# Performance work log

Measured on AMD Instinct MI355X. Metric: run time of the kernel, lower is better.

## Reference

```python
import jax, jax.numpy as jnp
import numpy as np

B, S, D, K = 8, 2048, 1024, 256
LN_EPS = 1e-5


def _freq_positions(input_dim, num_freq, spec_len):
    # torch.linspace(0, input_dim//2, num_freq).long(), clamped to rfft length
    pos = np.linspace(0.0, input_dim // 2, num_freq).astype(np.int64)
    return np.clip(pos, 0, spec_len - 1)


def setup_inputs() -> dict:
    key = jax.random.key(0)
    k1, k2, k3 = jax.random.split(key, 3)
    x = jax.random.normal(k1, (B, S, D), dtype=jnp.float32)
    # magnitude init: init_magnitude=0.1 (small jitter keeps gradients non-degenerate)
    magnitude = 0.1 + 0.01 * jax.random.normal(k2, (K, D), dtype=jnp.float32)
    phase = 0.1 * jax.random.normal(k3, (K, D), dtype=jnp.float32)
    interference_w = 0.01 * jax.random.normal(jax.random.fold_in(key, 7), (K, K), dtype=jnp.float32)
    ln_gamma = jnp.ones((D,), dtype=jnp.float32)
    ln_beta = jnp.zeros((D,), dtype=jnp.float32)
    return {"x": x, "magnitude": magnitude, "phase": phase,
            "interference_w": interference_w, "ln_gamma": ln_gamma, "ln_beta": ln_beta}


def reference(x, magnitude, phase, interference_w, ln_gamma, ln_beta):
    b, s, d = x.shape
    residual = x
    padded_len = 1 << int(np.ceil(np.log2(s)))  # static
    if padded_len > s:
        x = jnp.pad(x, ((0, 0), (0, padded_len - s), (0, 0)))
    # FFT along sequence axis: (B, padded_len//2+1, D) complex
    x_fft = jnp.fft.rfft(x, axis=1)
    freq_pos = _freq_positions(d, magnitude.shape[0], x_fft.shape[1])  # (K,) static ints

    # gather selected frequencies: (B, K, D)
    x_selected = x_fft[:, freq_pos, :]
    # complex weights from magnitude/phase
    cw = (magnitude * jnp.cos(phase) + 1j * magnitude * jnp.sin(phase)).astype(jnp.complex64)
    x_weighted = x_selected * cw[None, :, :]
    # interference on real part: bkd,kj->bjd
    interference = jnp.einsum('bkd,kj->bjd', jnp.real(x_weighted), interference_w)
    x_processed = x_weighted + 0.1 * interference.astype(jnp.complex64)

    # scatter back (positions are unique for these dims)
    x_fft_processed = x_fft.at[:, freq_pos, :].set(x_processed)
    x_rec = jnp.fft.irfft(x_fft_processed, n=padded_len, axis=1)[:, :s, :]

    # residual + LayerNorm over last dim (dropout is identity in eval)
    y = x_rec + residual
    mu = jnp.mean(y, axis=-1, keepdims=True)
    var = jnp.mean(jnp.square(y - mu), axis=-1, keepdims=True)
    y = (y - mu) * jax.lax.rsqrt(var + LN_EPS)
    return y * ln_gamma + ln_beta
```

## Files before the change

kernel.cpp:

```cpp
#include <hip/hip_runtime.h>
#include <math.h>

#define NS 2048
#define ND 1024
#define NK 256
#define NB 8

typedef __attribute__((ext_vector_type(8))) short short8;
typedef __attribute__((ext_vector_type(4))) float f32x4;
typedef __attribute__((ext_vector_type(4))) unsigned short u16x4;
typedef __attribute__((ext_vector_type(8))) unsigned short u16x8;

__device__ __forceinline__ unsigned short f2bf(float x) {
  unsigned int u = __float_as_uint(x);
  u = (u + 0x7fffu + ((u >> 16) & 1u)) >> 16;
  return (unsigned short)u;
}
__device__ __forceinline__ float bf2f(unsigned short h) {
  return __uint_as_float(((unsigned int)h) << 16);
}

__device__ __forceinline__ int fpos(int k) {
  return (k == 255) ? 512 : (int)((float)k * (512.0f / 255.0f));
}

__global__ __launch_bounds__(256) void k_tab(unsigned short* __restrict__ CF,
                                             unsigned short* __restrict__ CS) {
  int gid = blockIdx.x * 256 + threadIdx.x;
  if (gid < 512 * 2048) {
    int m = gid >> 11, s = gid & 2047;
    int ph = (fpos(m & 255) * s) & 2047;
    float th = (float)ph * 0.0030679615757712823f;
    float v = (m < 256) ? cosf(th) : -sinf(th);
    CF[gid] = f2bf(v);
  } else {
    int g = gid - 512 * 2048;
    int s = g >> 9, kk = g & 511;
    int ph = (fpos(kk & 255) * s) & 2047;
    float th = (float)ph * 0.0030679615757712823f;
    float v = (kk < 256) ? cosf(th) : -sinf(th);
    CS[g] = f2bf(v);
  }
}

__global__ __launch_bounds__(256) void k_cw(const float* __restrict__ mag,
                                            const float* __restrict__ ph,
                                            float* __restrict__ mc,
                                            float* __restrict__ ms) {
  int i = blockIdx.x * 256 + threadIdx.x;
  float m = mag[i], p = ph[i];
  float sp, cp;
  sincosf(p, &sp, &cp);
  mc[i] = m * cp;
  ms[i] = m * sp;
}

__global__ __launch_bounds__(256) void k_conv(const float* __restrict__ x,
                                              unsigned short* __restrict__ xt) {
  int bid = blockIdx.x;
  int b = bid >> 9, rem = bid & 511;
  int s0 = (rem >> 4) * 64, d0 = (rem & 15) * 64;
  int t = threadIdx.x;
  __shared__ __attribute__((aligned(16))) unsigned short lt[64 * 72];
#pragma unroll
  for (int c = 0; c < 4; c++) {
    int e = c * 256 + t;
    int row = e >> 4, col = (e & 15) * 4;
    float4 v = *(const float4*)&x[((size_t)b * NS + s0 + row) * ND + d0 + col];
    lt[(col + 0) * 72 + row] = f2bf(v.x);
    lt[(col + 1) * 72 + row] = f2bf(v.y);
    lt[(col + 2) * 72 + row] = f2bf(v.z);
    lt[(col + 3) * 72 + row] = f2bf(v.w);
  }
  __syncthreads();
  int dl = t >> 2, sc = (t & 3) * 16;
  u16x8 a = *(u16x8*)&lt[dl * 72 + sc];
  u16x8 bb = *(u16x8*)&lt[dl * 72 + sc + 8];
  size_t o = ((size_t)b * ND + d0 + dl) * NS + s0 + sc;
  *(u16x8*)&xt[o] = a;
  *(u16x8*)&xt[o + 8] = bb;
}

template <int BM, int BN, int OUTBF>
__global__ __launch_bounds__(256) void gemm_tt(const unsigned short* __restrict__ A,
                                               const unsigned short* __restrict__ B,
                                               void* __restrict__ C,
                                               int M, int N, int K) {
  constexpr int MI = BM / 32, NI = BN / 32;
  constexpr int ACH = BM / 32, BCH = BN / 32;
  const int mt = M / BM, nt = N / BN;
  int bid = blockIdx.x;
  int b = bid / (mt * nt);
  int r = bid % (mt * nt);
  int m0 = (r / nt) * BM, n0 = (r % nt) * BN;
  int t = threadIdx.x, lane = t & 63;
  int wr = (t >> 7) & 1, wc = (t >> 6) & 1;
  __shared__ __attribute__((aligned(16))) unsigned short As[BM * 64];
  __shared__ __attribute__((aligned(16))) unsigned short Bs[BN * 64];

  const unsigned short* Ag = A + (size_t)m0 * K;
  const unsigned short* Bg = B + ((size_t)b * N + n0) * K;

  f32x4 acc[MI][NI];
#pragma unroll
  for (int i = 0; i < MI; i++)
#pragma unroll
    for (int j = 0; j < NI; j++) acc[i][j] = {0.f, 0.f, 0.f, 0.f};

  short8 la[ACH], lb[BCH], na[ACH], nb[BCH];

#pragma unroll
  for (int c = 0; c < ACH; c++) {
    int e = c * 256 + t, row = e >> 3, sl = e & 7;
    la[c] = *(const short8*)&Ag[(size_t)row * K + sl * 8];
  }
#pragma unroll
  for (int c = 0; c < BCH; c++) {
    int e = c * 256 + t, row = e >> 3, sl = e & 7;
    lb[c] = *(const short8*)&Bg[(size_t)row * K + sl * 8];
  }

  const int nkt = K / 64;
  for (int kt = 0; kt < nkt; ++kt) {
    if (kt + 1 < nkt) {
      int k0 = (kt + 1) * 64;
#pragma unroll
      for (int c = 0; c < ACH; c++) {
        int e = c * 256 + t, row = e >> 3, sl = e & 7;
        na[c] = *(const short8*)&Ag[(size_t)row * K + k0 + sl * 8];
      }
#pragma unroll
      for (int c = 0; c < BCH; c++) {
        int e = c * 256 + t, row = e >> 3, sl = e & 7;
        nb[c] = *(const short8*)&Bg[(size_t)row * K + k0 + sl * 8];
      }
    }
    __syncthreads();
#pragma unroll
    for (int c = 0; c < ACH; c++) {
      int e = c * 256 + t, row = e >> 3, sl = e & 7;
      *(short8*)&As[row * 64 + ((sl ^ (row & 7)) * 8)] = la[c];
    }
#pragma unroll
    for (int c = 0; c < BCH; c++) {
      int e = c * 256 + t, row = e >> 3, sl = e & 7;
      *(short8*)&Bs[row * 64 + ((sl ^ (row & 7)) * 8)] = lb[c];
    }
    __syncthreads();
#pragma unroll
    for (int ks = 0; ks < 2; ks++) {
      short8 af[MI], bfr[NI];
#pragma unroll
      for (int mi = 0; mi < MI; mi++) {
        int rowl = wr * (BM / 2) + mi * 16 + (lane & 15);
        int sl = ks * 4 + (lane >> 4);
        af[mi] = *(const short8*)&As[rowl * 64 + ((sl ^ (rowl & 7)) * 8)];
      }
#pragma unroll
      for (int ni = 0; ni < NI; ni++) {
        int rowl = wc * (BN / 2) + ni * 16 + (lane & 15);
        int sl = ks * 4 + (lane >> 4);
        bfr[ni] = *(const short8*)&Bs[rowl * 64 + ((sl ^ (rowl & 7)) * 8)];
      }
#pragma unroll
      for (int mi = 0; mi < MI; mi++)
#pragma unroll
        for (int ni = 0; ni < NI; ni++)
          acc[mi][ni] = __builtin_amdgcn_mfma_f32_16x16x32_bf16(
              af[mi], bfr[ni], acc[mi][ni], 0, 0, 0);
    }
#pragma unroll
    for (int c = 0; c < ACH; c++) la[c] = na[c];
#pragma unroll
    for (int c = 0; c < BCH; c++) lb[c] = nb[c];
  }

#pragma unroll
  for (int mi = 0; mi < MI; mi++) {
#pragma unroll
    for (int ni = 0; ni < NI; ni++) {
      int row0 = m0 + wr * (BM / 2) + mi * 16 + ((lane >> 4) * 4);
      int col = n0 + wc * (BN / 2) + ni * 16 + (lane & 15);
#pragma unroll
      for (int q = 0; q < 4; q++) {
        size_t o = ((size_t)b * M + row0 + q) * (size_t)N + col;
        if (OUTBF)
          ((unsigned short*)C)[o] = f2bf(acc[mi][ni][q]);
        else
          ((float*)C)[o] = acc[mi][ni][q];
      }
    }
  }
}

__global__ __launch_bounds__(256) void k1b(const unsigned short* __restrict__ Xq,
                                           const float* __restrict__ mc,
                                           const float* __restrict__ ms,
                                           unsigned short* __restrict__ RXw) {
  int e8 = blockIdx.x * 256 + threadIdx.x;
  int d8 = (e8 & 127) * 8;
  int rowg = e8 >> 7;
  int b = rowg >> 8, k = rowg & 255;
  u16x8 re = *(const u16x8*)&Xq[((size_t)b * 512 + k) * ND + d8];
  u16x8 im = *(const u16x8*)&Xq[((size_t)b * 512 + 256 + k) * ND + d8];
  u16x8 o;
#pragma unroll
  for (int q = 0; q < 8; q++) {
    float mcv = mc[k * ND + d8 + q], msv = ms[k * ND + d8 + q];
    o[q] = f2bf(mcv * bf2f(re[q]) - msv * bf2f(im[q]));
  }
  *(u16x8*)&RXw[(size_t)rowg * ND + d8] = o;
}

__global__ __launch_bounds__(256) void k2_intf(const float* __restrict__ W,
                                               const unsigned short* __restrict__ RXw,
                                               const unsigned short* __restrict__ Xq,
                                               const float* __restrict__ mc,
                                               const float* __restrict__ ms,
                                               unsigned short* __restrict__ DltT) {
  int bid = blockIdx.x;
  int b = bid >> 6, rem = bid & 63;
  int jt = rem >> 4, dt = rem & 15;
  int t = threadIdx.x;
  int tj = t >> 4, td = t & 15;
  __shared__ __attribute__((aligned(16))) unsigned short Rx[256 * 64];
  __shared__ __attribute__((aligned(16))) unsigned short Wl[256 * 64];
#pragma unroll
  for (int c = 0; c < 8; c++) {
    int e = c * 256 + t, row = e >> 3, col = (e & 7) * 8;
    *(u16x8*)&Rx[row * 64 + col] =
        *(const u16x8*)&RXw[((size_t)b * NK + row) * ND + dt * 64 + col];
  }
#pragma unroll
  for (int c = 0; c < 16; c++) {
    int e = c * 256 + t, row = e >> 4, col = (e & 15) * 4;
    float4 w = *(const float4*)&W[row * NK + jt * 64 + col];
    u16x4 wv = {f2bf(w.x), f2bf(w.y), f2bf(w.z), f2bf(w.w)};
    *(u16x4*)&Wl[row * 64 + col] = wv;
  }
  __syncthreads();
  float acc[4][4];
#pragma unroll
  for (int i = 0; i < 4; i++)
#pragma unroll
    for (int j = 0; j < 4; j++) acc[i][j] = 0.f;
#pragma unroll 4
  for (int k = 0; k < 256; k++) {
    u16x4 r4 = *(const u16x4*)&Rx[k * 64 + td * 4];
    u16x4 w4 = *(const u16x4*)&Wl[k * 64 + tj * 4];
    float rf[4] = {bf2f(r4[0]), bf2f(r4[1]), bf2f(r4[2]), bf2f(r4[3])};
    float wf[4] = {bf2f(w4[0]), bf2f(w4[1]), bf2f(w4[2]), bf2f(w4[3])};
#pragma unroll
    for (int jj = 0; jj < 4; jj++)
#pragma unroll
      for (int q = 0; q < 4; q++) acc[jj][q] = fmaf(wf[jj], rf[q], acc[jj][q]);
  }
  int jbase = jt * 64 + tj * 4;
  jbase = jt * 64 + tj * 4;
  int dg = dt * 64 + td * 4;
  float dre[4][4], dim[4][4];
#pragma unroll
  for (int jj = 0; jj < 4; jj++) {
    int j = jbase + jj;
    float alpha = ((j == 0) ? 1.0f : 2.0f) * (1.0f / 2048.0f);
    u16x4 re4 = *(const u16x4*)&Xq[((size_t)b * 512 + j) * ND + dg];
    u16x4 im4 = *(const u16x4*)&Xq[((size_t)b * 512 + 256 + j) * ND + dg];
    float4 mc4 = *(const float4*)&mc[j * ND + dg];
    float4 ms4 = *(const float4*)&ms[j * ND + dg];
    float mcc[4] = {mc4.x, mc4.y, mc4.z, mc4.w};
    float mss[4] = {ms4.x, ms4.y, ms4.z, ms4.w};
#pragma unroll
    for (int q = 0; q < 4; q++) {
      float xr = bf2f(re4[q]), xi = bf2f(im4[q]);
      float m1 = mcc[q] - 1.0f;
      dre[jj][q] = alpha * (m1 * xr - mss[q] * xi + 0.1f * acc[jj][q]);
      dim[jj][q] = alpha * (mss[q] * xr + m1 * xi);
    }
  }
#pragma unroll
  for (int q = 0; q < 4; q++) {
    u16x4 vr = {f2bf(dre[0][q]), f2bf(dre[1][q]), f2bf(dre[2][q]), f2bf(dre[3][q])};
    u16x4 vi = {f2bf(dim[0][q]), f2bf(dim[1][q]), f2bf(dim[2][q]), f2bf(dim[3][q])};
    size_t rowo = ((size_t)b * ND + dg + q) * 512;
    *(u16x4*)&DltT[rowo + jbase] = vr;
    *(u16x4*)&DltT[rowo + 256 + jbase] = vi;
  }
}

__global__ __launch_bounds__(256) void k4_ln(const float* __restrict__ x,
                                             const float* __restrict__ g,
                                             const float* __restrict__ be,
                                             float* __restrict__ out) {
  int row = blockIdx.x;
  int t = threadIdx.x;
  size_t base = (size_t)row * ND + t * 4;
  float4 cv = *(float4*)&out[base];
  float4 xv = *(const float4*)&x[base];
  float v[4] = {fmaf(2.f, xv.x, cv.x), fmaf(2.f, xv.y, cv.y),
                fmaf(2.f, xv.z, cv.z), fmaf(2.f, xv.w, cv.w)};
  float s = v[0] + v[1] + v[2] + v[3];
  float q = v[0] * v[0] + v[1] * v[1] + v[2] * v[2] + v[3] * v[3];
#pragma unroll
  for (int o = 32; o >= 1; o >>= 1) {
    s += __shfl_xor(s, o, 64);
    q += __shfl_xor(q, o, 64);
  }
  __shared__ float ss[4], qs[4];
  if ((t & 63) == 0) { ss[t >> 6] = s; qs[t >> 6] = q; }
  __syncthreads();
  s = ss[0] + ss[1] + ss[2] + ss[3];
  q = qs[0] + qs[1] + qs[2] + qs[3];
  float mu = s * (1.0f / (float)ND);
  float var = q * (1.0f / (float)ND) - mu * mu;
  float rstd = rsqrtf(var + 1e-5f);
  float4 gv = *(const float4*)&g[t * 4];
  float4 bv = *(const float4*)&be[t * 4];
  float4 ov;
  ov.x = (v[0] - mu) * rstd * gv.x + bv.x;
  ov.y = (v[1] - mu) * rstd * gv.y + bv.y;
  ov.z = (v[2] - mu) * rstd * gv.z + bv.z;
  ov.w = (v[3] - mu) * rstd * gv.w + bv.w;
  *(float4*)&out[base] = ov;
}

extern "C" void kernel_launch(void* const* d_in, const int* in_sizes, int n_in,
                              void* d_out, int out_size, void* d_ws, size_t ws_size,
                              hipStream_t stream) {
  const float* x   = (const float*)d_in[0];
  const float* mag = (const float*)d_in[1];
  const float* ph  = (const float*)d_in[2];
  const float* W   = (const float*)d_in[3];
  const float* g   = (const float*)d_in[4];
  const float* be  = (const float*)d_in[5];
  float* out = (float*)d_out;
  char* o = (char*)d_out;
  char* w = (char*)d_ws;

  unsigned short* CF  = (unsigned short*)w;
  unsigned short* CS  = (unsigned short*)(w + (2u << 20));
  float* mc           = (float*)(w + (4u << 20));
  float* ms           = (float*)(w + (5u << 20));
  unsigned short* Dlt = (unsigned short*)(w + (6u << 20));
  unsigned short* xt  = (unsigned short*)o;
  unsigned short* Xq  = (unsigned short*)(o + (32u << 20));
  unsigned short* RXw = (unsigned short*)(o + (40u << 20));

  k_tab<<<8192, 256, 0, stream>>>(CF, CS);
  k_cw<<<1024, 256, 0, stream>>>(mag, ph, mc, ms);
  k_conv<<<4096, 256, 0, stream>>>(x, xt);
  gemm_tt<128, 64, 1><<<512, 256, 0, stream>>>(CF, xt, Xq, 512, 1024, 2048);
  k1b<<<1024, 256, 0, stream>>>(Xq, mc, ms, RXw);
  k2_intf<<<512, 256, 0, stream>>>(W, RXw, Xq, mc, ms, Dlt);
  gemm_tt<128, 128, 0><<<1024, 256, 0, stream>>>(CS, Dlt, out, 2048, 1024, 512);
  k4_ln<<<16384, 256, 0, stream>>>(x, g, be, out);
}
```

Measured before the change: 242.3 us.

## Transpose spectral intermediates, use MFMA for interference, direct-to-LDS GEMM loads

Reorganizes the pipeline so the forward DFT GEMM writes its output transposed (d-major), with the weight tables and interference matrix pre-transposed to match. The scalar FMA interference kernel is replaced by an MFMA GEMM plus a separate elementwise kernel. The GEMM is rewritten to use global_load_lds instead of register staging, which drops the XOR swizzle and the software prefetch. The inverse GEMM now writes a bf16 correction buffer rather than fp32, which cuts memory traffic but adds rounding error, and the unswizzled LDS layout may cause bank conflicts.

```diff
diff --git a/kernel.cpp b/kernel.cpp
--- a/kernel.cpp
+++ b/kernel.cpp
@@ -22,6 +22,12 @@
 
 __device__ __forceinline__ int fpos(int k) {
   return (k == 255) ? 512 : (int)((float)k * (512.0f / 255.0f));
+}
+
+__device__ __forceinline__ void gll16(const unsigned short* g, unsigned short* l) {
+  __builtin_amdgcn_global_load_lds(
+      (__attribute__((address_space(1))) void*)(void*)const_cast<unsigned short*>(g),
+      (__attribute__((address_space(3))) void*)l, 16, 0, 0);
 }
 
 __global__ __launch_bounds__(256) void k_tab(unsigned short* __restrict__ CF,
@@ -43,16 +49,64 @@
   }
 }
 
-__global__ __launch_bounds__(256) void k_cw(const float* __restrict__ mag,
-                                            const float* __restrict__ ph,
-                                            float* __restrict__ mc,
-                                            float* __restrict__ ms) {
-  int i = blockIdx.x * 256 + threadIdx.x;
-  float m = mag[i], p = ph[i];
-  float sp, cp;
-  sincosf(p, &sp, &cp);
-  mc[i] = m * cp;
-  ms[i] = m * sp;
+__global__ __launch_bounds__(256) void k_cwT(const float* __restrict__ mag,
+                                             const float* __restrict__ ph,
+                                             float* __restrict__ mcT,
+                                             float* __restrict__ msT) {
+  int bid = blockIdx.x;
+  int kt = bid >> 4, dt = bid & 15;
+  int t = threadIdx.x;
+  __shared__ float lc[64][68], ls[64][68];
+  int kl = t >> 4, d4 = (t & 15) * 4;
+#pragma unroll
+  for (int i = 0; i < 4; i++) {
+    int k = i * 16 + kl;
+    size_t off = (size_t)(kt * 64 + k) * ND + dt * 64 + d4;
+    float4 mg = *(const float4*)&mag[off];
+    float4 pp = *(const float4*)&ph[off];
+    float m[4] = {mg.x, mg.y, mg.z, mg.w}, p[4] = {pp.x, pp.y, pp.z, pp.w};
+#pragma unroll
+    for (int q = 0; q < 4; q++) {
+      float sp, cp;
+      sincosf(p[q], &sp, &cp);
+      lc[k][d4 + q] = m[q] * cp;
+      ls[k][d4 + q] = m[q] * sp;
+    }
+  }
+  __syncthreads();
+  int dl = t >> 2, kc = (t & 3) * 16;
+#pragma unroll
+  for (int i = 0; i < 16; i += 4) {
+    float4 vc = {lc[kc + i][dl], lc[kc + i + 1][dl], lc[kc + i + 2][dl], lc[kc + i + 3][dl]};
+    float4 vs = {ls[kc + i][dl], ls[kc + i + 1][dl], ls[kc + i + 2][dl], ls[kc + i + 3][dl]};
+    size_t o = (size_t)(dt * 64 + dl) * 256 + kt * 64 + kc + i;
+    *(float4*)&mcT[o] = vc;
+    *(float4*)&msT[o] = vs;
+  }
+}
+
+__global__ __launch_bounds__(256) void k_wt(const float* __restrict__ W,
+                                            unsigned short* __restrict__ WT) {
+  int bid = blockIdx.x;
+  int kt = bid >> 2, jt = bid & 3;
+  int t = threadIdx.x;
+  __shared__ float lw[64][68];
+  int kl = t >> 4, j4 = (t & 15) * 4;
+#pragma unroll
+  for (int i = 0; i < 4; i++) {
+    int k = i * 16 + kl;
+    float4 wv = *(const float4*)&W[(size_t)(kt * 64 + k) * 256 + jt * 64 + j4];
+    lw[k][j4 + 0] = wv.x; lw[k][j4 + 1] = wv.y;
+    lw[k][j4 + 2] = wv.z; lw[k][j4 + 3] = wv.w;
+  }
+  __syncthreads();
+  int jl = t >> 2, kc = (t & 3) * 16;
+#pragma unroll
+  for (int i = 0; i < 16; i += 4) {
+    u16x4 v = {f2bf(lw[kc + i][jl]), f2bf(lw[kc + i + 1][jl]),
+               f2bf(lw[kc + i + 2][jl]), f2bf(lw[kc + i + 3][jl])};
+    *(u16x4*)&WT[(size_t)(jt * 64 + jl) * 256 + kt * 64 + kc + i] = v;
+  }
 }
 
 __global__ __launch_bounds__(256) void k_conv(const float* __restrict__ x,
@@ -81,25 +135,24 @@
   *(u16x8*)&xt[o + 8] = bb;
 }
 
-template <int BM, int BN, int OUTBF>
-__global__ __launch_bounds__(256) void gemm_tt(const unsigned short* __restrict__ A,
-                                               const unsigned short* __restrict__ B,
-                                               void* __restrict__ C,
-                                               int M, int N, int K) {
+template <int BM, int BN, int OUTT>
+__global__ __launch_bounds__(256) void gemm97(const unsigned short* __restrict__ A,
+                                              const unsigned short* __restrict__ B,
+                                              unsigned short* __restrict__ C,
+                                              int M, int N, int K,
+                                              size_t sA, size_t sB) {
   constexpr int MI = BM / 32, NI = BN / 32;
-  constexpr int ACH = BM / 32, BCH = BN / 32;
   const int mt = M / BM, nt = N / BN;
   int bid = blockIdx.x;
-  int b = bid / (mt * nt);
-  int r = bid % (mt * nt);
+  int b = bid / (mt * nt), r = bid % (mt * nt);
   int m0 = (r / nt) * BM, n0 = (r % nt) * BN;
-  int t = threadIdx.x, lane = t & 63;
+  int t = threadIdx.x, lane = t & 63, w = t >> 6;
   int wr = (t >> 7) & 1, wc = (t >> 6) & 1;
   __shared__ __attribute__((aligned(16))) unsigned short As[BM * 64];
   __shared__ __attribute__((aligned(16))) unsigned short Bs[BN * 64];
-
-  const unsigned short* Ag = A + (size_t)m0 * K;
-  const unsigned short* Bg = B + ((size_t)b * N + n0) * K;
+  const unsigned short* Ag = A + b * sA + (size_t)m0 * K;
+  const unsigned short* Bg = B + b * sB + (size_t)n0 * K;
+  int arow = lane >> 3, ak = (lane & 7) * 8;
 
   f32x4 acc[MI][NI];
 #pragma unroll
@@ -107,72 +160,40 @@
 #pragma unroll
     for (int j = 0; j < NI; j++) acc[i][j] = {0.f, 0.f, 0.f, 0.f};
 
-  short8 la[ACH], lb[BCH], na[ACH], nb[BCH];
-
-#pragma unroll
-  for (int c = 0; c < ACH; c++) {
-    int e = c * 256 + t, row = e >> 3, sl = e & 7;
-    la[c] = *(const short8*)&Ag[(size_t)row * K + sl * 8];
-  }
-#pragma unroll
-  for (int c = 0; c < BCH; c++) {
-    int e = c * 256 + t, row = e >> 3, sl = e & 7;
-    lb[c] = *(const short8*)&Bg[(size_t)row * K + sl * 8];
-  }
-
-  const int nkt = K / 64;
-  for (int kt = 0; kt < nkt; ++kt) {
-    if (kt + 1 < nkt) {
-      int k0 = (kt + 1) * 64;
-#pragma unroll
-      for (int c = 0; c < ACH; c++) {
-        int e = c * 256 + t, row = e >> 3, sl = e & 7;
-        na[c] = *(const short8*)&Ag[(size_t)row * K + k0 + sl * 8];
+  for (int kt = 0; kt < K / 64; kt++) {
+    int kofs = kt * 64;
+#pragma unroll
+    for (int i = 0; i < BM / 32; i++) {
+      int r0 = w * (BM / 4) + i * 8;
+      gll16(Ag + (size_t)(r0 + arow) * K + kofs + ak, &As[r0 * 64]);
+    }
+#pragma unroll
+    for (int i = 0; i < BN / 32; i++) {
+      int r0 = w * (BN / 4) + i * 8;
+      gll16(Bg + (size_t)(r0 + arow) * K + kofs + ak, &Bs[r0 * 64]);
+    }
+    __syncthreads();
+#pragma unroll
+    for (int ks = 0; ks < 2; ks++) {
+      short8 af[MI], bfv[NI];
+#pragma unroll
+      for (int mi = 0; mi < MI; mi++) {
+        int row = wr * (BM / 2) + mi * 16 + (lane & 15);
+        af[mi] = *(const short8*)&As[row * 64 + (ks * 4 + (lane >> 4)) * 8];
       }
 #pragma unroll
-      for (int c = 0; c < BCH; c++) {
-        int e = c * 256 + t, row = e >> 3, sl = e & 7;
-        nb[c] = *(const short8*)&Bg[(size_t)row * K + k0 + sl * 8];
-      }
-    }
-    __syncthreads();
-#pragma unroll
-    for (int c = 0; c < ACH; c++) {
-      int e = c * 256 + t, row = e >> 3, sl = e & 7;
-      *(short8*)&As[row * 64 + ((sl ^ (row & 7)) * 8)] = la[c];
-    }
-#pragma unroll
-    for (int c = 0; c < BCH; c++) {
-      int e = c * 256 + t, row = e >> 3, sl = e & 7;
-      *(short8*)&Bs[row * 64 + ((sl ^ (row & 7)) * 8)] = lb[c];
-    }
-    __syncthreads();
-#pragma unroll
-    for (int ks = 0; ks < 2; ks++) {
-      short8 af[MI], bfr[NI];
-#pragma unroll
-      for (int mi = 0; mi < MI; mi++) {
-        int rowl = wr * (BM / 2) + mi * 16 + (lane & 15);
-        int sl = ks * 4 + (lane >> 4);
-        af[mi] = *(const short8*)&As[rowl * 64 + ((sl ^ (rowl & 7)) * 8)];
-      }
-#pragma unroll
       for (int ni = 0; ni < NI; ni++) {
-        int rowl = wc * (BN / 2) + ni * 16 + (lane & 15);
-        int sl = ks * 4 + (lane >> 4);
-        bfr[ni] = *(const short8*)&Bs[rowl * 64 + ((sl ^ (rowl & 7)) * 8)];
+        int row = wc * (BN / 2) + ni * 16 + (lane & 15);
+        bfv[ni] = *(const short8*)&Bs[row * 64 + (ks * 4 + (lane >> 4)) * 8];
       }
 #pragma unroll
       for (int mi = 0; mi < MI; mi++)
 #pragma unroll
         for (int ni = 0; ni < NI; ni++)
           acc[mi][ni] = __builtin_amdgcn_mfma_f32_16x16x32_bf16(
-              af[mi], bfr[ni], acc[mi][ni], 0, 0, 0);
-    }
-#pragma unroll
-    for (int c = 0; c < ACH; c++) la[c] = na[c];
-#pragma unroll
-    for (int c = 0; c < BCH; c++) lb[c] = nb[c];
+              af[mi], bfv[ni], acc[mi][ni], 0, 0, 0);
+    }
+    __syncthreads();
   }
 
 #pragma unroll
@@ -181,123 +202,86 @@
     for (int ni = 0; ni < NI; ni++) {
       int row0 = m0 + wr * (BM / 2) + mi * 16 + ((lane >> 4) * 4);
       int col = n0 + wc * (BN / 2) + ni * 16 + (lane & 15);
-#pragma unroll
-      for (int q = 0; q < 4; q++) {
-        size_t o = ((size_t)b * M + row0 + q) * (size_t)N + col;
-        if (OUTBF)
-          ((unsigned short*)C)[o] = f2bf(acc[mi][ni][q]);
-        else
-          ((float*)C)[o] = acc[mi][ni][q];
+      if (OUTT == 1) {
+        u16x4 v = {f2bf(acc[mi][ni][0]), f2bf(acc[mi][ni][1]),
+                   f2bf(acc[mi][ni][2]), f2bf(acc[mi][ni][3])};
+        *(u16x4*)&C[((size_t)b * N + col) * M + row0] = v;
+      } else {
+#pragma unroll
+        for (int q = 0; q < 4; q++)
+          C[((size_t)b * M + row0 + q) * N + col] = f2bf(acc[mi][ni][q]);
       }
     }
   }
 }
 
-__global__ __launch_bounds__(256) void k1b(const unsigned short* __restrict__ Xq,
-                                           const float* __restrict__ mc,
-                                           const float* __restrict__ ms,
-                                           unsigned short* __restrict__ RXw) {
-  int e8 = blockIdx.x * 256 + threadIdx.x;
-  int d8 = (e8 & 127) * 8;
-  int rowg = e8 >> 7;
-  int b = rowg >> 8, k = rowg & 255;
-  u16x8 re = *(const u16x8*)&Xq[((size_t)b * 512 + k) * ND + d8];
-  u16x8 im = *(const u16x8*)&Xq[((size_t)b * 512 + 256 + k) * ND + d8];
+__global__ __launch_bounds__(256) void k1bT(const unsigned short* __restrict__ XqT,
+                                            const float* __restrict__ mcT,
+                                            const float* __restrict__ msT,
+                                            unsigned short* __restrict__ RXwT) {
+  int gid = blockIdx.x * 256 + threadIdx.x;
+  int rw = gid >> 5;
+  int k0 = (gid & 31) * 8;
+  int d = rw & 1023;
+  u16x8 re = *(const u16x8*)&XqT[(size_t)rw * 512 + k0];
+  u16x8 im = *(const u16x8*)&XqT[(size_t)rw * 512 + 256 + k0];
+  float4 c0 = *(const float4*)&mcT[d * 256 + k0];
+  float4 c1 = *(const float4*)&mcT[d * 256 + k0 + 4];
+  float4 s0 = *(const float4*)&msT[d * 256 + k0];
+  float4 s1 = *(const float4*)&msT[d * 256 + k0 + 4];
+  float cc[8] = {c0.x, c0.y, c0.z, c0.w, c1.x, c1.y, c1.z, c1.w};
+  float ss[8] = {s0.x, s0.y, s0.z, s0.w, s1.x, s1.y, s1.z, s1.w};
   u16x8 o;
 #pragma unroll
+  for (int q = 0; q < 8; q++)
+    o[q] = f2bf(cc[q] * bf2f(re[q]) - ss[q] * bf2f(im[q]));
+  *(u16x8*)&RXwT[(size_t)rw * 256 + k0] = o;
+}
+
+__global__ __launch_bounds__(256) void k2b(const unsigned short* __restrict__ IT,
+                                           const unsigned short* __restrict__ XqT,
+                                           const float* __restrict__ mcT,
+                                           const float* __restrict__ msT,
+                                           unsigned short* __restrict__ DltT) {
+  int gid = blockIdx.x * 256 + threadIdx.x;
+  int rw = gid >> 5;
+  int j0 = (gid & 31) * 8;
+  int d = rw & 1023;
+  u16x8 iv = *(const u16x8*)&IT[(size_t)rw * 256 + j0];
+  u16x8 re = *(const u16x8*)&XqT[(size_t)rw * 512 + j0];
+  u16x8 im = *(const u16x8*)&XqT[(size_t)rw * 512 + 256 + j0];
+  float4 c0 = *(const float4*)&mcT[d * 256 + j0];
+  float4 c1 = *(const float4*)&mcT[d * 256 + j0 + 4];
+  float4 s0 = *(const float4*)&msT[d * 256 + j0];
+  float4 s1 = *(const float4*)&msT[d * 256 + j0 + 4];
+  float cc[8] = {c0.x, c0.y, c0.z, c0.w, c1.x, c1.y, c1.z, c1.w};
+  float ss[8] = {s0.x, s0.y, s0.z, s0.w, s1.x, s1.y, s1.z, s1.w};
+  u16x8 orv, oiv;
+#pragma unroll
   for (int q = 0; q < 8; q++) {
-    float mcv = mc[k * ND + d8 + q], msv = ms[k * ND + d8 + q];
-    o[q] = f2bf(mcv * bf2f(re[q]) - msv * bf2f(im[q]));
-  }
-  *(u16x8*)&RXw[(size_t)rowg * ND + d8] = o;
-}
-
-__global__ __launch_bounds__(256) void k2_intf(const float* __restrict__ W,
-                                               const unsigned short* __restrict__ RXw,
-                                               const unsigned short* __restrict__ Xq,
-                                               const float* __restrict__ mc,
-                                               const float* __restrict__ ms,
-                                               unsigned short* __restrict__ DltT) {
-  int bid = blockIdx.x;
-  int b = bid >> 6, rem = bid & 63;
-  int jt = rem >> 4, dt = rem & 15;
-  int t = threadIdx.x;
-  int tj = t >> 4, td = t & 15;
-  __shared__ __attribute__((aligned(16))) unsigned short Rx[256 * 64];
-  __shared__ __attribute__((aligned(16))) unsigned short Wl[256 * 64];
-#pragma unroll
-  for (int c = 0; c < 8; c++) {
-    int e = c * 256 + t, row = e >> 3, col = (e & 7) * 8;
-    *(u16x8*)&Rx[row * 64 + col] =
-        *(const u16x8*)&RXw[((size_t)b * NK + row) * ND + dt * 64 + col];
-  }
-#pragma unroll
-  for (int c = 0; c < 16; c++) {
-    int e = c * 256 + t, row = e >> 4, col = (e & 15) * 4;
-    float4 w = *(const float4*)&W[row * NK + jt * 64 + col];
-    u16x4 wv = {f2bf(w.x), f2bf(w.y), f2bf(w.z), f2bf(w.w)};
-    *(u16x4*)&Wl[row * 64 + col] = wv;
-  }
-  __syncthreads();
-  float acc[4][4];
-#pragma unroll
-  for (int i = 0; i < 4; i++)
-#pragma unroll
-    for (int j = 0; j < 4; j++) acc[i][j] = 0.f;
-#pragma unroll 4
-  for (int k = 0; k < 256; k++) {
-    u16x4 r4 = *(const u16x4*)&Rx[k * 64 + td * 4];
-    u16x4 w4 = *(const u16x4*)&Wl[k * 64 + tj * 4];
-    float rf[4] = {bf2f(r4[0]), bf2f(r4[1]), bf2f(r4[2]), bf2f(r4[3])};
-    float wf[4] = {bf2f(w4[0]), bf2f(w4[1]), bf2f(w4[2]), bf2f(w4[3])};
-#pragma unroll
-    for (int jj = 0; jj < 4; jj++)
-#pragma unroll
-      for (int q = 0; q < 4; q++) acc[jj][q] = fmaf(wf[jj], rf[q], acc[jj][q]);
-  }
-  int jbase = jt * 64 + tj * 4;
-  jbase = jt * 64 + tj * 4;
-  int dg = dt * 64 + td * 4;
-  float dre[4][4], dim[4][4];
-#pragma unroll
-  for (int jj = 0; jj < 4; jj++) {
-    int j = jbase + jj;
+    int j = j0 + q;
     float alpha = ((j == 0) ? 1.0f : 2.0f) * (1.0f / 2048.0f);
-    u16x4 re4 = *(const u16x4*)&Xq[((size_t)b * 512 + j) * ND + dg];
-    u16x4 im4 = *(const u16x4*)&Xq[((size_t)b * 512 + 256 + j) * ND + dg];
-    float4 mc4 = *(const float4*)&mc[j * ND + dg];
-    float4 ms4 = *(const float4*)&ms[j * ND + dg];
-    float mcc[4] = {mc4.x, mc4.y, mc4.z, mc4.w};
-    float mss[4] = {ms4.x, ms4.y, ms4.z, ms4.w};
-#pragma unroll
-    for (int q = 0; q < 4; q++) {
-      float xr = bf2f(re4[q]), xi = bf2f(im4[q]);
-      float m1 = mcc[q] - 1.0f;
-      dre[jj][q] = alpha * (m1 * xr - mss[q] * xi + 0.1f * acc[jj][q]);
-      dim[jj][q] = alpha * (mss[q] * xr + m1 * xi);
-    }
-  }
-#pragma unroll
-  for (int q = 0; q < 4; q++) {
-    u16x4 vr = {f2bf(dre[0][q]), f2bf(dre[1][q]), f2bf(dre[2][q]), f2bf(dre[3][q])};
-    u16x4 vi = {f2bf(dim[0][q]), f2bf(dim[1][q]), f2bf(dim[2][q]), f2bf(dim[3][q])};
-    size_t rowo = ((size_t)b * ND + dg + q) * 512;
-    *(u16x4*)&DltT[rowo + jbase] = vr;
-    *(u16x4*)&DltT[rowo + 256 + jbase] = vi;
-  }
+    float xr = bf2f(re[q]), xi = bf2f(im[q]), ii = bf2f(iv[q]);
+    float m1 = cc[q] - 1.0f;
+    orv[q] = f2bf(alpha * (m1 * xr - ss[q] * xi + 0.1f * ii));
+    oiv[q] = f2bf(alpha * (ss[q] * xr + m1 * xi));
+  }
+  *(u16x8*)&DltT[(size_t)rw * 512 + j0] = orv;
+  *(u16x8*)&DltT[(size_t)rw * 512 + 256 + j0] = oiv;
 }
 
 __global__ __launch_bounds__(256) void k4_ln(const float* __restrict__ x,
+                                             const unsigned short* __restrict__ corr,
                                              const float* __restrict__ g,
                                              const float* __restrict__ be,
                                              float* __restrict__ out) {
   int row = blockIdx.x;
   int t = threadIdx.x;
   size_t base = (size_t)row * ND + t * 4;
-  float4 cv = *(float4*)&out[base];
+  u16x4 cv = *(const u16x4*)&corr[base];
   float4 xv = *(const float4*)&x[base];
-  float v[4] = {fmaf(2.f, xv.x, cv.x), fmaf(2.f, xv.y, cv.y),
-                fmaf(2.f, xv.z, cv.z), fmaf(2.f, xv.w, cv.w)};
+  float v[4] = {fmaf(2.f, xv.x, bf2f(cv[0])), fmaf(2.f, xv.y, bf2f(cv[1])),
+                fmaf(2.f, xv.z, bf2f(cv[2])), fmaf(2.f, xv.w, bf2f(cv[3]))};
   float s = v[0] + v[1] + v[2] + v[3];
   float q = v[0] * v[0] + v[1] * v[1] + v[2] * v[2] + v[3] * v[3];
 #pragma unroll
@@ -333,24 +317,31 @@
   const float* g   = (const float*)d_in[4];
   const float* be  = (const float*)d_in[5];
   float* out = (float*)d_out;
-  char* o = (char*)d_out;
   char* w = (char*)d_ws;
 
-  unsigned short* CF  = (unsigned short*)w;
-  unsigned short* CS  = (unsigned short*)(w + (2u << 20));
-  float* mc           = (float*)(w + (4u << 20));
-  float* ms           = (float*)(w + (5u << 20));
-  unsigned short* Dlt = (unsigned short*)(w + (6u << 20));
-  unsigned short* xt  = (unsigned short*)o;
-  unsigned short* Xq  = (unsigned short*)(o + (32u << 20));
-  unsigned short* RXw = (unsigned short*)(o + (40u << 20));
+  unsigned short* CF   = (unsigned short*)(w);
+  unsigned short* CS   = (unsigned short*)(w + (2ull << 20));
+  float*          mcT  = (float*)(w + (4ull << 20));
+  float*          msT  = (float*)(w + (5ull << 20));
+  unsigned short* WT   = (unsigned short*)(w + (6ull << 20));
+  unsigned short* XqT  = (unsigned short*)(w + (7ull << 20));
+  unsigned short* RXwT = (unsigned short*)(w + (15ull << 20));
+  unsigned short* IT   = (unsigned short*)(w + (19ull << 20));
+  unsigned short* DltT = (unsigned short*)(w + (23ull << 20));
+  unsigned short* corr = (unsigned short*)(w + (31ull << 20));
+  unsigned short* xt   = (unsigned short*)(w + (63ull << 20));
 
   k_tab<<<8192, 256, 0, stream>>>(CF, CS);
-  k_cw<<<1024, 256, 0, stream>>>(mag, ph, mc, ms);
+  k_cwT<<<64, 256, 0, stream>>>(mag, ph, mcT, msT);
+  k_wt<<<16, 256, 0, stream>>>(W, WT);
   k_conv<<<4096, 256, 0, stream>>>(x, xt);
-  gemm_tt<128, 64, 1><<<512, 256, 0, stream>>>(CF, xt, Xq, 512, 1024, 2048);
-  k1b<<<1024, 256, 0, stream>>>(Xq, mc, ms, RXw);
-  k2_intf<<<512, 256, 0, stream>>>(W, RXw, Xq, mc, ms, Dlt);
-  gemm_tt<128, 128, 0><<<1024, 256, 0, stream>>>(CS, Dlt, out, 2048, 1024, 512);
-  k4_ln<<<16384, 256, 0, stream>>>(x, g, be, out);
-}
+  gemm97<128, 64, 1><<<512, 256, 0, stream>>>(CF, xt, XqT, 512, 1024, 2048,
+                                              0, (size_t)1024 * 2048);
+  k1bT<<<1024, 256, 0, stream>>>(XqT, mcT, msT, RXwT);
+  gemm97<128, 64, 0><<<256, 256, 0, stream>>>(RXwT, WT, IT, 1024, 256, 256,
+                                              (size_t)1024 * 256, 0);
+  k2b<<<1024, 256, 0, stream>>>(IT, XqT, mcT, msT, DltT);
+  gemm97<128, 128, 0><<<1024, 256, 0, stream>>>(CS, DltT, corr, 2048, 1024, 512,
+                                                0, (size_t)1024 * 512);
+  k4_ln<<<16384, 256, 0, stream>>>(x, corr, g, be, out);
+}
```

Result: no change. 239.4 us (-1.2%).
